# Kernel tuning notes

Measured on AMD Instinct MI355X. Metric: run time of the kernel, lower is better.

The kernel has to match this reference:

```python
import jax, jax.numpy as jnp
import numpy as np

N, E, F_IN, H, L, E_FEAT, G, OUT = 100000, 1600000, 8, 128, 4, 16, 256, 256


def setup_inputs() -> dict:
    key = jax.random.key(0)
    ks = jax.random.split(key, 12)
    inp = {
        "x": jax.random.normal(ks[0], (N, F_IN), jnp.float32),
        "edge_index": jax.random.randint(ks[1], (2, E), 0, N),
        "edge_attr": jax.random.uniform(ks[2], (E, E_FEAT), jnp.float32),
        "batch": jnp.sort(jax.random.randint(ks[3], (N,), 0, G)),
        "emb_W": jax.random.normal(ks[4], (F_IN, H), jnp.float32) / np.sqrt(F_IN),
        "emb_b": jnp.zeros((H,), jnp.float32),
        "edge_W": jax.random.normal(ks[5], (L, E_FEAT, H), jnp.float32) / np.sqrt(E_FEAT),
        "edge_b": jnp.zeros((L, H), jnp.float32),
        "nn_W": jax.random.normal(ks[6], (L, H, H), jnp.float32) / np.sqrt(H),
        "nn_b": jnp.zeros((L, H), jnp.float32),
        "bn_g": jnp.ones((L, H), jnp.float32),
        "bn_b": jnp.zeros((L, H), jnp.float32),
        "lin_W": jax.random.normal(ks[7], (H, OUT), jnp.float32) / np.sqrt(H),
        "lin_b": jnp.zeros((OUT,), jnp.float32),
    }
    return inp


def reference(x, edge_index, edge_attr, batch, emb_W, emb_b, edge_W, edge_b,
              nn_W, nn_b, bn_g, bn_b, lin_W, lin_b):
    eps_bn = 1e-5
    src, dst = edge_index[0], edge_index[1]
    h = x @ emb_W + emb_b  # node embedding [N,H]
    for l in range(L):
        e = edge_attr @ edge_W[l] + edge_b[l]          # [E,H] edge embedding
        msg = jax.nn.relu(h[src] + e)                   # gather + message
        agg = jax.ops.segment_sum(msg, dst, num_segments=N)  # scatter-add
        hc = (h + agg) @ nn_W[l] + nn_b[l]             # GINE nn (eps=0)
        mu = jnp.mean(hc, axis=0)
        var = jnp.mean((hc - mu) ** 2, axis=0)          # biased var (train BN)
        hc = (hc - mu) * jax.lax.rsqrt(var + eps_bn) * bn_g[l] + bn_b[l]
        hc = jax.nn.gelu(hc, approximate=False)
        h = h + hc                                      # 'res' residual
    out = h @ lin_W + lin_b                             # [N,OUT]
    rep = jax.ops.segment_sum(out, batch, num_segments=G)  # global_add_pool
    return rep
```

## Files before the change

### kernel.cpp

```cpp
#include <hip/hip_runtime.h>
#include <hip/hip_fp16.h>
#include <math.h>

#define GG 256

typedef __attribute__((ext_vector_type(8))) short short8;
typedef __attribute__((ext_vector_type(4))) float f32x4;
typedef _Float16 half2v __attribute__((ext_vector_type(2)));
typedef __attribute__((ext_vector_type(4))) unsigned uint4v;
typedef __attribute__((ext_vector_type(8))) unsigned uint8v;

__device__ __forceinline__ unsigned short f2bf(float x) {
  union { float f; unsigned u; } v; v.f = x;
  unsigned r = v.u + 0x7fff + ((v.u >> 16) & 1);
  return (unsigned short)(r >> 16);
}

__device__ __forceinline__ unsigned pack_h2(float a, float b) {
  __half2 h = __floats2half2_rn(a, b);
  return *(unsigned*)&h;
}

__device__ __forceinline__ float fdot2u(unsigned a, unsigned b, float c) {
  half2v av, bv;
  __builtin_memcpy(&av, &a, 4);
  __builtin_memcpy(&bv, &b, 4);
  return __builtin_amdgcn_fdot2(av, bv, c, false);
}

__device__ __forceinline__ uint4v sload4(const void* p) {
  uint4v r;
  asm volatile("s_load_dwordx4 %0, %1, 0x0"
               : "=s"(r) : "s"((unsigned long long)p));
  return r;
}
__device__ __forceinline__ uint8v sload8(const void* p) {
  uint8v r;
  asm volatile("s_load_dwordx8 %0, %1, 0x0"
               : "=s"(r) : "s"((unsigned long long)p));
  return r;
}
__device__ __forceinline__ void swait() {
  asm volatile("s_waitcnt lgkmcnt(0)" ::: "memory");
  __builtin_amdgcn_sched_barrier(0);
}

__global__ __launch_bounds__(256) void k_emb(const float* __restrict__ x,
    const float* __restrict__ W, const float* __restrict__ b,
    float* __restrict__ h, unsigned short* __restrict__ hb, int N) {
  int idx = blockIdx.x * 256 + threadIdx.x;
  if (idx >= N * 32) return;
  int n = idx >> 5, q = idx & 31;
  const float* xr = x + (size_t)n * 8;
  float xs[8];
#pragma unroll
  for (int k = 0; k < 8; ++k) xs[k] = xr[k];
  float4 acc = ((const float4*)b)[q];
#pragma unroll
  for (int k = 0; k < 8; ++k) {
    float4 w = ((const float4*)(W + (size_t)k * 128))[q];
    acc.x += xs[k] * w.x; acc.y += xs[k] * w.y;
    acc.z += xs[k] * w.z; acc.w += xs[k] * w.w;
  }
  ((float4*)h)[idx] = acc;
  ushort4 hv4 = make_ushort4(f2bf(acc.x), f2bf(acc.y), f2bf(acc.z), f2bf(acc.w));
  *(ushort4*)(hb + (size_t)idx * 4) = hv4;
}

__global__ __launch_bounds__(256) void k_wconv(const float* __restrict__ eW,
    unsigned* __restrict__ eWp) {
  int i = blockIdx.x * 256 + threadIdx.x;
  if (i >= 4096) return;
  int c = i & 127, k = (i >> 7) & 7, l = i >> 10;
  const float* base = eW + ((size_t)(l * 16 + 2 * k) * 128 + c);
  eWp[i] = pack_h2(base[0], base[128]);
}

__global__ __launch_bounds__(256) void k_nnconv(const float* __restrict__ W,
    unsigned short* __restrict__ WT) {
  int i = blockIdx.x * 256 + threadIdx.x;
  if (i >= 4 * 128 * 128) return;
  int n = i & 127, k = (i >> 7) & 127, l = i >> 14;
  WT[((size_t)(l * 128 + n)) * 128 + k] = f2bf(W[i]);
}

__global__ void k_hist(const int* __restrict__ dst, int* __restrict__ deg, int E) {
  int e = blockIdx.x * blockDim.x + threadIdx.x;
  if (e < E) atomicAdd(&deg[dst[e]], 1);
}

__global__ __launch_bounds__(256) void k_scan_reduce(const int* __restrict__ deg,
    int* __restrict__ bsum, int N) {
  __shared__ int sd[256];
  int i = blockIdx.x * 256 + threadIdx.x;
  sd[threadIdx.x] = (i < N) ? deg[i] : 0;
  __syncthreads();
  for (int s = 128; s > 0; s >>= 1) {
    if (threadIdx.x < s) sd[threadIdx.x] += sd[threadIdx.x + s];
    __syncthreads();
  }
  if (threadIdx.x == 0) bsum[blockIdx.x] = sd[0];
}

__global__ __launch_bounds__(512) void k_scan_mid(int* bsum, int nb) {
  __shared__ int sd[512];
  int t = threadIdx.x;
  int v = (t < nb) ? bsum[t] : 0;
  sd[t] = v; __syncthreads();
  for (int d = 1; d < 512; d <<= 1) {
    int xv = (t >= d) ? sd[t - d] : 0;
    __syncthreads();
    sd[t] += xv;
    __syncthreads();
  }
  if (t < nb) bsum[t] = sd[t] - v;
}

__global__ __launch_bounds__(256) void k_scan_final(const int* __restrict__ deg,
    const int* __restrict__ bsum, int* __restrict__ offs,
    int* __restrict__ cursor, int N) {
  __shared__ int sd[256];
  int t = threadIdx.x;
  int i = blockIdx.x * 256 + t;
  int v = (i < N) ? deg[i] : 0;
  sd[t] = v; __syncthreads();
  for (int d = 1; d < 256; d <<= 1) {
    int xv = (t >= d) ? sd[t - d] : 0;
    __syncthreads();
    sd[t] += xv;
    __syncthreads();
  }
  int off = bsum[blockIdx.x] + sd[t] - v;
  if (i < N) {
    offs[i] = off; cursor[i] = off;
    if (i == N - 1) offs[N] = off + v;
  }
}

__global__ void k_fill(const int* __restrict__ src, const int* __restrict__ dst,
    const float* __restrict__ attr, int* __restrict__ cursor,
    int* __restrict__ csrc, uint4* __restrict__ cattr16, int E) {
  int e = blockIdx.x * blockDim.x + threadIdx.x;
  if (e >= E) return;
  int d = dst[e];
  int pos = atomicAdd(&cursor[d], 1);
  csrc[pos] = src[e];
  const float4* a = (const float4*)(attr + (size_t)e * 16);
  float4 a0 = a[0], a1 = a[1], a2 = a[2], a3 = a[3];
  uint4 o0, o1;
  o0.x = pack_h2(a0.x, a0.y); o0.y = pack_h2(a0.z, a0.w);
  o0.z = pack_h2(a1.x, a1.y); o0.w = pack_h2(a1.z, a1.w);
  o1.x = pack_h2(a2.x, a2.y); o1.y = pack_h2(a2.z, a2.w);
  o1.z = pack_h2(a3.x, a3.y); o1.w = pack_h2(a3.z, a3.w);
  cattr16[(size_t)pos * 2] = o0;
  cattr16[(size_t)pos * 2 + 1] = o1;
}

__global__ void k_gstart(const int* __restrict__ batch, int* __restrict__ gstart,
                         int N, int Gn) {
  int i = blockIdx.x * blockDim.x + threadIdx.x;
  if (i >= N) return;
  int b = batch[i];
  if (i == 0) { for (int g = 0; g <= b; ++g) gstart[g] = 0; }
  else { int bp = batch[i - 1]; for (int g = bp + 1; g <= b; ++g) gstart[g] = i; }
  if (i == N - 1) { for (int g = b + 1; g <= Gn; ++g) gstart[g] = N; }
}

__global__ __launch_bounds__(256) void k_edge_agg(const float* __restrict__ h,
    const unsigned* __restrict__ hb32,
    const uint4* __restrict__ cattr16, const int* __restrict__ csrc,
    const int* __restrict__ offs, const unsigned* __restrict__ eWp,
    const float* __restrict__ eb, unsigned* __restrict__ hpa16,
    float* __restrict__ cstats, int N) {
  int t = threadIdx.x;
  if (blockIdx.x == 0) cstats[t] = 0.f;
  int l = t & 63;
  int wid = blockIdx.x * 4 + (t >> 6);
  int nw = gridDim.x * 4;
  uint2 wp[8];
#pragma unroll
  for (int k = 0; k < 8; ++k) wp[k] = *(const uint2*)&eWp[k * 128 + 2 * l];
  float2 bias = *(const float2*)(eb + 2 * l);
  const unsigned* hb_l = hb32 + l;

#define EDGE_SG(A, UU, AX, AY)                                              \
  {                                                                         \
    float e0 = bias.x, e1 = bias.y;                                         \
    e0 = fdot2u(A[0], wp[0].x, e0); e1 = fdot2u(A[0], wp[0].y, e1);         \
    e0 = fdot2u(A[1], wp[1].x, e0); e1 = fdot2u(A[1], wp[1].y, e1);         \
    e0 = fdot2u(A[2], wp[2].x, e0); e1 = fdot2u(A[2], wp[2].y, e1);         \
    e0 = fdot2u(A[3], wp[3].x, e0); e1 = fdot2u(A[3], wp[3].y, e1);         \
    e0 = fdot2u(A[4], wp[4].x, e0); e1 = fdot2u(A[4], wp[4].y, e1);         \
    e0 = fdot2u(A[5], wp[5].x, e0); e1 = fdot2u(A[5], wp[5].y, e1);         \
    e0 = fdot2u(A[6], wp[6].x, e0); e1 = fdot2u(A[6], wp[6].y, e1);         \
    e0 = fdot2u(A[7], wp[7].x, e0); e1 = fdot2u(A[7], wp[7].y, e1);         \
    union { unsigned uu; float ff; } c0, c1;                                \
    c0.uu = (UU) << 16; c1.uu = (UU) & 0xffff0000u;                         \
    AX += fmaxf(e0 + c0.ff, 0.f);                                           \
    AY += fmaxf(e1 + c1.ff, 0.f);                                           \
  }

#define EDGE2(JJ, UU, AX, AY)                                               \
  {                                                                         \
    uint4 q0 = cattr16[(size_t)(JJ) * 2];                                   \
    uint4 q1 = cattr16[(size_t)(JJ) * 2 + 1];                               \
    float e0 = bias.x, e1 = bias.y;                                         \
    e0 = fdot2u(q0.x, wp[0].x, e0); e1 = fdot2u(q0.x, wp[0].y, e1);         \
    e0 = fdot2u(q0.y, wp[1].x, e0); e1 = fdot2u(q0.y, wp[1].y, e1);         \
    e0 = fdot2u(q0.z, wp[2].x, e0); e1 = fdot2u(q0.z, wp[2].y, e1);         \
    e0 = fdot2u(q0.w, wp[3].x, e0); e1 = fdot2u(q0.w, wp[3].y, e1);         \
    e0 = fdot2u(q1.x, wp[4].x, e0); e1 = fdot2u(q1.x, wp[4].y, e1);         \
    e0 = fdot2u(q1.y, wp[5].x, e0); e1 = fdot2u(q1.y, wp[5].y, e1);         \
    e0 = fdot2u(q1.z, wp[6].x, e0); e1 = fdot2u(q1.z, wp[6].y, e1);         \
    e0 = fdot2u(q1.w, wp[7].x, e0); e1 = fdot2u(q1.w, wp[7].y, e1);         \
    union { unsigned uu; float ff; } c0, c1;                                \
    c0.uu = (UU) << 16; c1.uu = (UU) & 0xffff0000u;                         \
    AX += fmaxf(e0 + c0.ff, 0.f);                                           \
    AY += fmaxf(e1 + c1.ff, 0.f);                                           \
  }

  for (int n = wid; n < N; n += nw) {
    int jb = offs[n], je = offs[n + 1];
    jb = __builtin_amdgcn_readfirstlane(jb);
    je = __builtin_amdgcn_readfirstlane(je);
    float ax = 0.f, ay = 0.f, bx = 0.f, by = 0.f;
    int j = jb;
    for (; j + 4 <= je; j += 4) {
      const char* ab = (const char*)cattr16 + ((unsigned long long)(unsigned)j << 5);
      uint4v sc = sload4((const char*)csrc + ((unsigned long long)(unsigned)j << 2));
      uint8v A0 = sload8(ab);
      uint8v A1 = sload8(ab + 32);
      uint8v A2 = sload8(ab + 64);
      uint8v A3 = sload8(ab + 96);
      swait();
      const unsigned* r0 = (const unsigned*)((const char*)hb32 + ((unsigned long long)sc[0] << 8));
      const unsigned* r1 = (const unsigned*)((const char*)hb32 + ((unsigned long long)sc[1] << 8));
      const unsigned* r2 = (const unsigned*)((const char*)hb32 + ((unsigned long long)sc[2] << 8));
      const unsigned* r3 = (const unsigned*)((const char*)hb32 + ((unsigned long long)sc[3] << 8));
      unsigned u0 = r0[l], u1 = r1[l], u2 = r2[l], u3 = r3[l];
      EDGE_SG(A0, u0, ax, ay)
      EDGE_SG(A1, u1, bx, by)
      EDGE_SG(A2, u2, ax, ay)
      EDGE_SG(A3, u3, bx, by)
    }
    for (; j < je; ++j) {
      int s0 = csrc[j];
      unsigned u0 = hb_l[(size_t)s0 * 64];
      EDGE2(j, u0, ax, ay)
    }
    float2 hvv = *(const float2*)(h + (size_t)n * 128 + 2 * l);
    float rx = hvv.x + ax + bx;
    float ry = hvv.y + ay + by;
    hpa16[(size_t)n * 64 + l] = ((unsigned)f2bf(ry) << 16) | (unsigned)f2bf(rx);
  }
#undef EDGE_SG
#undef EDGE2
}

__global__ __launch_bounds__(256) void k_gemm_mfma(
    const unsigned short* __restrict__ A16, const unsigned short* __restrict__ WT16,
    const float* __restrict__ bias, float* __restrict__ hc,
    float* __restrict__ cstats, int N) {
  __shared__ short a_lds[128 * 136];
  __shared__ short w_lds[128 * 136];
  int t = threadIdx.x;
  int rowbase = blockIdx.x * 128;
  {
    int r = t >> 1;
    int off = (t & 1) * 64;
    const short* ga = (const short*)A16 + (size_t)(rowbase + r) * 128 + off;
    short* la = &a_lds[r * 136 + off];
    const short* gw = (const short*)WT16 + (size_t)r * 128 + off;
    short* lw = &w_lds[r * 136 + off];
    if (rowbase + r < N) {
#pragma unroll
      for (int jj = 0; jj < 8; ++jj)
        *(uint4*)(la + jj * 8) = *(const uint4*)(ga + jj * 8);
    } else {
#pragma unroll
      for (int jj = 0; jj < 8; ++jj)
        *(uint4*)(la + jj * 8) = make_uint4(0, 0, 0, 0);
    }
#pragma unroll
    for (int jj = 0; jj < 8; ++jj)
      *(uint4*)(lw + jj * 8) = *(const uint4*)(gw + jj * 8);
  }
  __syncthreads();
  int w = t >> 6;
  int lane = t & 63;
  int l15 = lane & 15, quad = lane >> 4;
  f32x4 acc[2][8];
#pragma unroll
  for (int rt = 0; rt < 2; ++rt)
#pragma unroll
    for (int nt = 0; nt < 8; ++nt)
      acc[rt][nt] = (f32x4){0.f, 0.f, 0.f, 0.f};
#pragma unroll
  for (int kc = 0; kc < 4; ++kc) {
    int k0 = kc * 32 + quad * 8;
    short8 af0 = *(const short8*)&a_lds[(w * 32 + l15) * 136 + k0];
    short8 af1 = *(const short8*)&a_lds[(w * 32 + 16 + l15) * 136 + k0];
#pragma unroll
    for (int nt = 0; nt < 8; ++nt) {
      short8 bf = *(const short8*)&w_lds[(nt * 16 + l15) * 136 + k0];
      acc[0][nt] = __builtin_amdgcn_mfma_f32_16x16x32_bf16(af0, bf, acc[0][nt], 0, 0, 0);
      acc[1][nt] = __builtin_amdgcn_mfma_f32_16x16x32_bf16(af1, bf, acc[1][nt], 0, 0, 0);
    }
  }
  float sA[8], sQ[8];
#pragma unroll
  for (int nt = 0; nt < 8; ++nt) { sA[nt] = 0.f; sQ[nt] = 0.f; }
#pragma unroll
  for (int nt = 0; nt < 8; ++nt) {
    int col = nt * 16 + l15;
    float bv = bias[col];
#pragma unroll
    for (int rt = 0; rt < 2; ++rt) {
      int rbase = rowbase + w * 32 + rt * 16 + quad * 4;
#pragma unroll
      for (int reg = 0; reg < 4; ++reg) {
        int row = rbase + reg;
        float v = acc[rt][nt][reg] + bv;
        if (row < N) {
          hc[(size_t)row * 128 + col] = v;
          sA[nt] += v; sQ[nt] += v * v;
        }
      }
    }
  }
#pragma unroll
  for (int nt = 0; nt < 8; ++nt) {
    sA[nt] += __shfl_xor(sA[nt], 16);
    sA[nt] += __shfl_xor(sA[nt], 32);
    sQ[nt] += __shfl_xor(sQ[nt], 16);
    sQ[nt] += __shfl_xor(sQ[nt], 32);
  }
  __syncthreads();
  float* sdA = (float*)a_lds;
  float* sdQ = (float*)w_lds;
  if (quad == 0) {
#pragma unroll
    for (int nt = 0; nt < 8; ++nt) {
      sdA[w * 128 + nt * 16 + l15] = sA[nt];
      sdQ[w * 128 + nt * 16 + l15] = sQ[nt];
    }
  }
  __syncthreads();
  if (t < 128) {
    float s = sdA[t] + sdA[128 + t] + sdA[256 + t] + sdA[384 + t];
    float s2 = sdQ[t] + sdQ[128 + t] + sdQ[256 + t] + sdQ[384 + t];
    atomicAdd(&cstats[t], s);
    atomicAdd(&cstats[128 + t], s2);
  }
}

__global__ __launch_bounds__(256) void k_bn(const float* __restrict__ hc,
    const float* __restrict__ cstats,
    const float* __restrict__ g, const float* __restrict__ bb,
    float* __restrict__ h, unsigned short* __restrict__ hb, int N) {
  int idx = blockIdx.x * 256 + threadIdx.x;
  if (idx >= N * 32) return;
  int q = idx & 31;
  float invN = 1.f / (float)N;
  float4 cs = ((const float4*)cstats)[q];
  float4 cq = ((const float4*)cstats)[q + 32];
  float4 gv = ((const float4*)g)[q];
  float4 bv = ((const float4*)bb)[q];
  float4 v = ((const float4*)hc)[idx];
  float4 hv = ((const float4*)h)[idx];
#define BN1(X)                                                      \
  { float mu = cs.X * invN;                                         \
    float var = cq.X * invN - mu * mu;                              \
    float xn = (v.X - mu) * rsqrtf(var + 1e-5f) * gv.X + bv.X;      \
    hv.X += 0.5f * xn * (1.f + erff(xn * 0.70710678118654752f)); }
  BN1(x) BN1(y) BN1(z) BN1(w)
#undef BN1
  ((float4*)h)[idx] = hv;
  if (hb) {
    ushort4 hv4 = make_ushort4(f2bf(hv.x), f2bf(hv.y), f2bf(hv.z), f2bf(hv.w));
    *(ushort4*)(hb + (size_t)idx * 4) = hv4;
  }
}

__global__ __launch_bounds__(256) void k_poolfinal(const float* __restrict__ h,
    const int* __restrict__ gstart, const float* __restrict__ W,
    const float* __restrict__ b, float* __restrict__ out) {
  int g = blockIdx.x;
  int t = threadIdx.x, c = t & 127, half = t >> 7;
  int n0 = gstart[g], n1 = gstart[g + 1];
  float s = 0.f;
  for (int n = n0 + half; n < n1; n += 2) s += h[(size_t)n * 128 + c];
  __shared__ float ls[256];
  __shared__ float pr[128];
  ls[t] = s; __syncthreads();
  if (t < 128) pr[t] = ls[t] + ls[t + 128];
  __syncthreads();
  float cnt = (float)(n1 - n0);
  float acc = cnt * b[t];
#pragma unroll 8
  for (int k = 0; k < 128; ++k) acc += pr[k] * W[(size_t)k * 256 + t];
  out[(size_t)g * 256 + t] = acc;
}

extern "C" void kernel_launch(void* const* d_in, const int* in_sizes, int n_in,
                              void* d_out, int out_size, void* d_ws, size_t ws_size,
                              hipStream_t stream) {
  const float* x     = (const float*)d_in[0];
  const int*   eidx  = (const int*)d_in[1];
  const float* eattr = (const float*)d_in[2];
  const int*   batch = (const int*)d_in[3];
  const float* embW  = (const float*)d_in[4];
  const float* embB  = (const float*)d_in[5];
  const float* edgeW = (const float*)d_in[6];
  const float* edgeB = (const float*)d_in[7];
  const float* nnW   = (const float*)d_in[8];
  const float* nnB   = (const float*)d_in[9];
  const float* bnG   = (const float*)d_in[10];
  const float* bnB   = (const float*)d_in[11];
  const float* linW  = (const float*)d_in[12];
  const float* linB  = (const float*)d_in[13];
  float* out = (float*)d_out;

  int N = in_sizes[0] / 8;
  int E = in_sizes[1] / 2;
  const int* src = eidx;
  const int* dst = eidx + E;

  char* wptr = (char*)d_ws;
  auto alloc = [&](size_t bytes) {
    char* p = wptr; wptr += (bytes + 255) & ~(size_t)255; return p;
  };
  float* h      = (float*)alloc((size_t)N * 128 * 4);
  float* hc     = (float*)alloc((size_t)N * 128 * 4);
  unsigned short* hb = (unsigned short*)alloc((size_t)N * 128 * 2);
  unsigned* hpa16 = (unsigned*)alloc((size_t)N * 64 * 4);
  uint4* cattr16 = (uint4*)alloc((size_t)E * 32);
  int*   csrc   = (int*)alloc((size_t)E * 4);
  int*   offs   = (int*)alloc((size_t)(N + 1) * 4);
  int*   cursor = (int*)alloc((size_t)N * 4);
  int*   deg    = (int*)alloc((size_t)N * 4);
  int nb = (N + 255) / 256;
  int*   bsum   = (int*)alloc((size_t)nb * 4);
  float* cstats = (float*)alloc(256 * 4);
  unsigned* eW16 = (unsigned*)alloc(4096 * 4);
  unsigned short* WT16 = (unsigned short*)alloc(4 * 128 * 128 * 2);
  int*   gstart = (int*)alloc((size_t)(GG + 1) * 4);

  int q32 = (N * 32 + 255) / 256;

  hipMemsetAsync(deg, 0, (size_t)N * 4, stream);
  k_emb<<<q32, 256, 0, stream>>>(x, embW, embB, h, hb, N);
  k_wconv<<<16, 256, 0, stream>>>(edgeW, eW16);
  k_nnconv<<<256, 256, 0, stream>>>(nnW, WT16);
  k_hist<<<(E + 255) / 256, 256, 0, stream>>>(dst, deg, E);
  k_scan_reduce<<<nb, 256, 0, stream>>>(deg, bsum, N);
  k_scan_mid<<<1, 512, 0, stream>>>(bsum, nb);
  k_scan_final<<<nb, 256, 0, stream>>>(deg, bsum, offs, cursor, N);
  k_fill<<<(E + 255) / 256, 256, 0, stream>>>(src, dst, eattr, cursor, csrc, cattr16, E);
  k_gstart<<<(N + 255) / 256, 256, 0, stream>>>(batch, gstart, N, GG);

  int gblk = (N + 127) / 128;
  for (int l = 0; l < 4; ++l) {
    k_edge_agg<<<8192, 256, 0, stream>>>(h, (const unsigned*)hb, cattr16, csrc,
        offs, eW16 + (size_t)l * 1024, edgeB + (size_t)l * 128, hpa16, cstats, N);
    k_gemm_mfma<<<gblk, 256, 0, stream>>>((const unsigned short*)hpa16,
        WT16 + (size_t)l * 128 * 128, nnB + (size_t)l * 128, hc, cstats, N);
    k_bn<<<q32, 256, 0, stream>>>(hc, cstats,
        bnG + (size_t)l * 128, bnB + (size_t)l * 128, h, (l == 3) ? nullptr : hb, N);
  }
  k_poolfinal<<<GG, 256, 0, stream>>>(h, gstart, linW, linB, out);
}
```

Baseline: 1.045 ms.

## Split CSR attr fill into coalesced convert, perm, and gather; vector-load edge attrs

Edge attribute fp16 conversion now runs as a separate coalesced pass. The CSR fill records only a permutation, and a third kernel gathers the packed 32-byte attrs into CSR order, replacing the scattered fp32 reads and writes inside the atomic fill. The scratch buffers reuse the hc and hpa16 workspace, which is enlarged when needed. In the edge aggregation kernel, attr loads move from scalar sload8 to per-lane vector loads, the loop unrolls by 8 edges with csrc prefetch, and launch bounds request 4 blocks per CU. This adds two extra kernel launches and a second pass over the attribute data.

```diff
diff --git a/kernel.cpp b/kernel.cpp
--- a/kernel.cpp
+++ b/kernel.cpp
@@ -82,6 +82,18 @@
   if (i >= 4 * 128 * 128) return;
   int n = i & 127, k = (i >> 7) & 127, l = i >> 14;
   WT[((size_t)(l * 128 + n)) * 128 + k] = f2bf(W[i]);
+}
+
+__global__ __launch_bounds__(256) void k_aconv(const float* __restrict__ attr,
+    uint4* __restrict__ attr16c, int E2) {
+  int i = blockIdx.x * 256 + threadIdx.x;
+  if (i >= E2) return;
+  float4 a0 = ((const float4*)attr)[(size_t)i * 2];
+  float4 a1 = ((const float4*)attr)[(size_t)i * 2 + 1];
+  uint4 o;
+  o.x = pack_h2(a0.x, a0.y); o.y = pack_h2(a0.z, a0.w);
+  o.z = pack_h2(a1.x, a1.y); o.w = pack_h2(a1.z, a1.w);
+  attr16c[i] = o;
 }
 
 __global__ void k_hist(const int* __restrict__ dst, int* __restrict__ deg, int E) {
@@ -137,23 +149,25 @@
   }
 }
 
-__global__ void k_fill(const int* __restrict__ src, const int* __restrict__ dst,
-    const float* __restrict__ attr, int* __restrict__ cursor,
-    int* __restrict__ csrc, uint4* __restrict__ cattr16, int E) {
+__global__ void k_fillperm(const int* __restrict__ src, const int* __restrict__ dst,
+    int* __restrict__ cursor, int* __restrict__ csrc, int* __restrict__ perm, int E) {
   int e = blockIdx.x * blockDim.x + threadIdx.x;
   if (e >= E) return;
   int d = dst[e];
   int pos = atomicAdd(&cursor[d], 1);
   csrc[pos] = src[e];
-  const float4* a = (const float4*)(attr + (size_t)e * 16);
-  float4 a0 = a[0], a1 = a[1], a2 = a[2], a3 = a[3];
-  uint4 o0, o1;
-  o0.x = pack_h2(a0.x, a0.y); o0.y = pack_h2(a0.z, a0.w);
-  o0.z = pack_h2(a1.x, a1.y); o0.w = pack_h2(a1.z, a1.w);
-  o1.x = pack_h2(a2.x, a2.y); o1.y = pack_h2(a2.z, a2.w);
-  o1.z = pack_h2(a3.x, a3.y); o1.w = pack_h2(a3.z, a3.w);
-  cattr16[(size_t)pos * 2] = o0;
-  cattr16[(size_t)pos * 2 + 1] = o1;
+  perm[pos] = e;
+}
+
+__global__ __launch_bounds__(256) void k_permgather(const int* __restrict__ perm,
+    const uint4* __restrict__ attr16c, uint4* __restrict__ cattr16, int E) {
+  int pos = blockIdx.x * 256 + threadIdx.x;
+  if (pos >= E) return;
+  int e = perm[pos];
+  uint4 a0 = attr16c[(size_t)e * 2];
+  uint4 a1 = attr16c[(size_t)e * 2 + 1];
+  cattr16[(size_t)pos * 2] = a0;
+  cattr16[(size_t)pos * 2 + 1] = a1;
 }
 
 __global__ void k_gstart(const int* __restrict__ batch, int* __restrict__ gstart,
@@ -166,7 +180,7 @@
   if (i == N - 1) { for (int g = b + 1; g <= Gn; ++g) gstart[g] = N; }
 }
 
-__global__ __launch_bounds__(256) void k_edge_agg(const float* __restrict__ h,
+__global__ __launch_bounds__(256, 4) void k_edge_agg(const float* __restrict__ h,
     const unsigned* __restrict__ hb32,
     const uint4* __restrict__ cattr16, const int* __restrict__ csrc,
     const int* __restrict__ offs, const unsigned* __restrict__ eWp,
@@ -177,84 +191,100 @@
   int l = t & 63;
   int wid = blockIdx.x * 4 + (t >> 6);
   int nw = gridDim.x * 4;
+  unsigned dz = __builtin_amdgcn_mbcnt_lo(0u, 0u);
   uint2 wp[8];
 #pragma unroll
   for (int k = 0; k < 8; ++k) wp[k] = *(const uint2*)&eWp[k * 128 + 2 * l];
   float2 bias = *(const float2*)(eb + 2 * l);
   const unsigned* hb_l = hb32 + l;
 
-#define EDGE_SG(A, UU, AX, AY)                                              \
+#define EDGE_V(P0, P1, UU, AX, AY)                                          \
   {                                                                         \
     float e0 = bias.x, e1 = bias.y;                                         \
-    e0 = fdot2u(A[0], wp[0].x, e0); e1 = fdot2u(A[0], wp[0].y, e1);         \
-    e0 = fdot2u(A[1], wp[1].x, e0); e1 = fdot2u(A[1], wp[1].y, e1);         \
-    e0 = fdot2u(A[2], wp[2].x, e0); e1 = fdot2u(A[2], wp[2].y, e1);         \
-    e0 = fdot2u(A[3], wp[3].x, e0); e1 = fdot2u(A[3], wp[3].y, e1);         \
-    e0 = fdot2u(A[4], wp[4].x, e0); e1 = fdot2u(A[4], wp[4].y, e1);         \
-    e0 = fdot2u(A[5], wp[5].x, e0); e1 = fdot2u(A[5], wp[5].y, e1);         \
-    e0 = fdot2u(A[6], wp[6].x, e0); e1 = fdot2u(A[6], wp[6].y, e1);         \
-    e0 = fdot2u(A[7], wp[7].x, e0); e1 = fdot2u(A[7], wp[7].y, e1);         \
+    e0 = fdot2u(P0.x, wp[0].x, e0); e1 = fdot2u(P0.x, wp[0].y, e1);         \
+    e0 = fdot2u(P0.y, wp[1].x, e0); e1 = fdot2u(P0.y, wp[1].y, e1);         \
+    e0 = fdot2u(P0.z, wp[2].x, e0); e1 = fdot2u(P0.z, wp[2].y, e1);         \
+    e0 = fdot2u(P0.w, wp[3].x, e0); e1 = fdot2u(P0.w, wp[3].y, e1);         \
+    e0 = fdot2u(P1.x, wp[4].x, e0); e1 = fdot2u(P1.x, wp[4].y, e1);         \
+    e0 = fdot2u(P1.y, wp[5].x, e0); e1 = fdot2u(P1.y, wp[5].y, e1);         \
+    e0 = fdot2u(P1.z, wp[6].x, e0); e1 = fdot2u(P1.z, wp[6].y, e1);         \
+    e0 = fdot2u(P1.w, wp[7].x, e0); e1 = fdot2u(P1.w, wp[7].y, e1);         \
     union { unsigned uu; float ff; } c0, c1;                                \
     c0.uu = (UU) << 16; c1.uu = (UU) & 0xffff0000u;                         \
     AX += fmaxf(e0 + c0.ff, 0.f);                                           \
     AY += fmaxf(e1 + c1.ff, 0.f);                                           \
   }
 
-#define EDGE2(JJ, UU, AX, AY)                                               \
-  {                                                                         \
-    uint4 q0 = cattr16[(size_t)(JJ) * 2];                                   \
-    uint4 q1 = cattr16[(size_t)(JJ) * 2 + 1];                               \
-    float e0 = bias.x, e1 = bias.y;                                         \
-    e0 = fdot2u(q0.x, wp[0].x, e0); e1 = fdot2u(q0.x, wp[0].y, e1);         \
-    e0 = fdot2u(q0.y, wp[1].x, e0); e1 = fdot2u(q0.y, wp[1].y, e1);         \
-    e0 = fdot2u(q0.z, wp[2].x, e0); e1 = fdot2u(q0.z, wp[2].y, e1);         \
-    e0 = fdot2u(q0.w, wp[3].x, e0); e1 = fdot2u(q0.w, wp[3].y, e1);         \
-    e0 = fdot2u(q1.x, wp[4].x, e0); e1 = fdot2u(q1.x, wp[4].y, e1);         \
-    e0 = fdot2u(q1.y, wp[5].x, e0); e1 = fdot2u(q1.y, wp[5].y, e1);         \
-    e0 = fdot2u(q1.z, wp[6].x, e0); e1 = fdot2u(q1.z, wp[6].y, e1);         \
-    e0 = fdot2u(q1.w, wp[7].x, e0); e1 = fdot2u(q1.w, wp[7].y, e1);         \
-    union { unsigned uu; float ff; } c0, c1;                                \
-    c0.uu = (UU) << 16; c1.uu = (UU) & 0xffff0000u;                         \
-    AX += fmaxf(e0 + c0.ff, 0.f);                                           \
-    AY += fmaxf(e1 + c1.ff, 0.f);                                           \
-  }
+#define LOADATTR(R0, R1, R2, R3, R4, R5, R6, R7, JJ)                        \
+  { const uint4* gp = cattr16 + (((size_t)(unsigned)(JJ)) << 1) + dz;       \
+    R0 = gp[0]; R1 = gp[1]; R2 = gp[2]; R3 = gp[3];                         \
+    R4 = gp[4]; R5 = gp[5]; R6 = gp[6]; R7 = gp[7]; }
+
+#define GATH(D, S)                                                          \
+  { const unsigned* rr = hb32 + ((size_t)(unsigned)(S)) * 64; D = rr[l]; }
 
   for (int n = wid; n < N; n += nw) {
-    int jb = offs[n], je = offs[n + 1];
-    jb = __builtin_amdgcn_readfirstlane(jb);
-    je = __builtin_amdgcn_readfirstlane(je);
+    int jb = __builtin_amdgcn_readfirstlane(offs[n]);
+    int je = __builtin_amdgcn_readfirstlane(offs[n + 1]);
     float ax = 0.f, ay = 0.f, bx = 0.f, by = 0.f;
     int j = jb;
-    for (; j + 4 <= je; j += 4) {
-      const char* ab = (const char*)cattr16 + ((unsigned long long)(unsigned)j << 5);
-      uint4v sc = sload4((const char*)csrc + ((unsigned long long)(unsigned)j << 2));
-      uint8v A0 = sload8(ab);
-      uint8v A1 = sload8(ab + 32);
-      uint8v A2 = sload8(ab + 64);
-      uint8v A3 = sload8(ab + 96);
+    if (j + 8 <= je) {
+      uint8v sc8 = sload8((const char*)csrc + ((size_t)(unsigned)j << 2));
       swait();
-      const unsigned* r0 = (const unsigned*)((const char*)hb32 + ((unsigned long long)sc[0] << 8));
-      const unsigned* r1 = (const unsigned*)((const char*)hb32 + ((unsigned long long)sc[1] << 8));
-      const unsigned* r2 = (const unsigned*)((const char*)hb32 + ((unsigned long long)sc[2] << 8));
-      const unsigned* r3 = (const unsigned*)((const char*)hb32 + ((unsigned long long)sc[3] << 8));
-      unsigned u0 = r0[l], u1 = r1[l], u2 = r2[l], u3 = r3[l];
-      EDGE_SG(A0, u0, ax, ay)
-      EDGE_SG(A1, u1, bx, by)
-      EDGE_SG(A2, u2, ax, ay)
-      EDGE_SG(A3, u3, bx, by)
+      for (;;) {
+        unsigned ua0, ua1, ua2, ua3, ub0, ub1, ub2, ub3;
+        uint4 Aa0, Aa1, Aa2, Aa3, Aa4, Aa5, Aa6, Aa7;
+        uint4 Ab0, Ab1, Ab2, Ab3, Ab4, Ab5, Ab6, Ab7;
+        GATH(ua0, sc8[0]) GATH(ua1, sc8[1]) GATH(ua2, sc8[2]) GATH(ua3, sc8[3])
+        LOADATTR(Aa0, Aa1, Aa2, Aa3, Aa4, Aa5, Aa6, Aa7, j)
+        GATH(ub0, sc8[4]) GATH(ub1, sc8[5]) GATH(ub2, sc8[6]) GATH(ub3, sc8[7])
+        LOADATTR(Ab0, Ab1, Ab2, Ab3, Ab4, Ab5, Ab6, Ab7, j + 4)
+        bool more = (j + 16 <= je);
+        uint8v sc8n;
+        if (more) sc8n = sload8((const char*)csrc + ((size_t)(unsigned)(j + 8) << 2));
+        EDGE_V(Aa0, Aa1, ua0, ax, ay)
+        EDGE_V(Aa2, Aa3, ua1, bx, by)
+        EDGE_V(Aa4, Aa5, ua2, ax, ay)
+        EDGE_V(Aa6, Aa7, ua3, bx, by)
+        EDGE_V(Ab0, Ab1, ub0, ax, ay)
+        EDGE_V(Ab2, Ab3, ub1, bx, by)
+        EDGE_V(Ab4, Ab5, ub2, ax, ay)
+        EDGE_V(Ab6, Ab7, ub3, bx, by)
+        j += 8;
+        if (!more) break;
+        swait();
+        sc8 = sc8n;
+      }
+    }
+    if (j + 4 <= je) {
+      uint4v sc4 = sload4((const char*)csrc + ((size_t)(unsigned)j << 2));
+      swait();
+      unsigned ua0, ua1, ua2, ua3;
+      uint4 Aa0, Aa1, Aa2, Aa3, Aa4, Aa5, Aa6, Aa7;
+      GATH(ua0, sc4[0]) GATH(ua1, sc4[1]) GATH(ua2, sc4[2]) GATH(ua3, sc4[3])
+      LOADATTR(Aa0, Aa1, Aa2, Aa3, Aa4, Aa5, Aa6, Aa7, j)
+      EDGE_V(Aa0, Aa1, ua0, ax, ay)
+      EDGE_V(Aa2, Aa3, ua1, bx, by)
+      EDGE_V(Aa4, Aa5, ua2, ax, ay)
+      EDGE_V(Aa6, Aa7, ua3, bx, by)
+      j += 4;
     }
     for (; j < je; ++j) {
       int s0 = csrc[j];
       unsigned u0 = hb_l[(size_t)s0 * 64];
-      EDGE2(j, u0, ax, ay)
+      uint4 P0, P1;
+      { const uint4* gp = cattr16 + (((size_t)(unsigned)j) << 1) + dz;
+        P0 = gp[0]; P1 = gp[1]; }
+      EDGE_V(P0, P1, u0, ax, ay)
     }
     float2 hvv = *(const float2*)(h + (size_t)n * 128 + 2 * l);
     float rx = hvv.x + ax + bx;
     float ry = hvv.y + ay + by;
     hpa16[(size_t)n * 64 + l] = ((unsigned)f2bf(ry) << 16) | (unsigned)f2bf(rx);
   }
-#undef EDGE_SG
-#undef EDGE2
+#undef EDGE_V
+#undef LOADATTR
+#undef GATH
 }
 
 __global__ __launch_bounds__(256) void k_gemm_mfma(
@@ -430,10 +460,14 @@
   auto alloc = [&](size_t bytes) {
     char* p = wptr; wptr += (bytes + 255) & ~(size_t)255; return p;
   };
+  size_t hc_bytes = (size_t)N * 128 * 4;
+  if ((size_t)E * 32 > hc_bytes) hc_bytes = (size_t)E * 32;
+  size_t hpa_bytes = (size_t)N * 64 * 4;
+  if ((size_t)E * 4 > hpa_bytes) hpa_bytes = (size_t)E * 4;
   float* h      = (float*)alloc((size_t)N * 128 * 4);
-  float* hc     = (float*)alloc((size_t)N * 128 * 4);
+  float* hc     = (float*)alloc(hc_bytes);
   unsigned short* hb = (unsigned short*)alloc((size_t)N * 128 * 2);
-  unsigned* hpa16 = (unsigned*)alloc((size_t)N * 64 * 4);
+  unsigned* hpa16 = (unsigned*)alloc(hpa_bytes);
   uint4* cattr16 = (uint4*)alloc((size_t)E * 32);
   int*   csrc   = (int*)alloc((size_t)E * 4);
   int*   offs   = (int*)alloc((size_t)(N + 1) * 4);
@@ -446,17 +480,22 @@
   unsigned short* WT16 = (unsigned short*)alloc(4 * 128 * 128 * 2);
   int*   gstart = (int*)alloc((size_t)(GG + 1) * 4);
 
+  uint4* attr16c = (uint4*)hc;
+  int*   perm    = (int*)hpa16;
+
   int q32 = (N * 32 + 255) / 256;
 
   hipMemsetAsync(deg, 0, (size_t)N * 4, stream);
   k_emb<<<q32, 256, 0, stream>>>(x, embW, embB, h, hb, N);
   k_wconv<<<16, 256, 0, stream>>>(edgeW, eW16);
   k_nnconv<<<256, 256, 0, stream>>>(nnW, WT16);
+  k_aconv<<<(E * 2 + 255) / 256, 256, 0, stream>>>(eattr, attr16c, E * 2);
   k_hist<<<(E + 255) / 256, 256, 0, stream>>>(dst, deg, E);
   k_scan_reduce<<<nb, 256, 0, stream>>>(deg, bsum, N);
   k_scan_mid<<<1, 512, 0, stream>>>(bsum, nb);
   k_scan_final<<<nb, 256, 0, stream>>>(deg, bsum, offs, cursor, N);
-  k_fill<<<(E + 255) / 256, 256, 0, stream>>>(src, dst, eattr, cursor, csrc, cattr16, E);
+  k_fillperm<<<(E + 255) / 256, 256, 0, stream>>>(src, dst, cursor, csrc, perm, E);
+  k_permgather<<<(E + 255) / 256, 256, 0, stream>>>(perm, attr16c, cattr16, E);
   k_gstart<<<(N + 255) / 256, 256, 0, stream>>>(batch, gstart, N, GG);
 
   int gblk = (N + 127) / 128;
```

After: 1.341 ms. +28.3%, slower.

## Double-buffer scalar loads of edge attributes and sources in edge aggregation

Applied to the files above, without the earlier changes.

Adds software pipelining to the edge-aggregation inner loop. While the current group of four edges is computed, the scalar loads for the next group of source indices and edge attributes are issued into a second register set (A/B ping-pong). The wider dwordx8 scalar loads are split into dwordx4 loads. The aim is to hide scalar-memory latency behind the gather and dot-product math, at the cost of higher SGPR pressure.

```diff
diff --git a/kernel.cpp b/kernel.cpp
--- a/kernel.cpp
+++ b/kernel.cpp
@@ -8,7 +8,6 @@
 typedef __attribute__((ext_vector_type(4))) float f32x4;
 typedef _Float16 half2v __attribute__((ext_vector_type(2)));
 typedef __attribute__((ext_vector_type(4))) unsigned uint4v;
-typedef __attribute__((ext_vector_type(8))) unsigned uint8v;
 
 __device__ __forceinline__ unsigned short f2bf(float x) {
   union { float f; unsigned u; } v; v.f = x;
@@ -31,12 +30,6 @@
 __device__ __forceinline__ uint4v sload4(const void* p) {
   uint4v r;
   asm volatile("s_load_dwordx4 %0, %1, 0x0"
-               : "=s"(r) : "s"((unsigned long long)p));
-  return r;
-}
-__device__ __forceinline__ uint8v sload8(const void* p) {
-  uint8v r;
-  asm volatile("s_load_dwordx8 %0, %1, 0x0"
                : "=s"(r) : "s"((unsigned long long)p));
   return r;
 }
@@ -183,17 +176,17 @@
   float2 bias = *(const float2*)(eb + 2 * l);
   const unsigned* hb_l = hb32 + l;
 
-#define EDGE_SG(A, UU, AX, AY)                                              \
+#define EDGE_SG(P, Q, UU, AX, AY)                                           \
   {                                                                         \
     float e0 = bias.x, e1 = bias.y;                                         \
-    e0 = fdot2u(A[0], wp[0].x, e0); e1 = fdot2u(A[0], wp[0].y, e1);         \
-    e0 = fdot2u(A[1], wp[1].x, e0); e1 = fdot2u(A[1], wp[1].y, e1);         \
-    e0 = fdot2u(A[2], wp[2].x, e0); e1 = fdot2u(A[2], wp[2].y, e1);         \
-    e0 = fdot2u(A[3], wp[3].x, e0); e1 = fdot2u(A[3], wp[3].y, e1);         \
-    e0 = fdot2u(A[4], wp[4].x, e0); e1 = fdot2u(A[4], wp[4].y, e1);         \
-    e0 = fdot2u(A[5], wp[5].x, e0); e1 = fdot2u(A[5], wp[5].y, e1);         \
-    e0 = fdot2u(A[6], wp[6].x, e0); e1 = fdot2u(A[6], wp[6].y, e1);         \
-    e0 = fdot2u(A[7], wp[7].x, e0); e1 = fdot2u(A[7], wp[7].y, e1);         \
+    e0 = fdot2u(P[0], wp[0].x, e0); e1 = fdot2u(P[0], wp[0].y, e1);         \
+    e0 = fdot2u(P[1], wp[1].x, e0); e1 = fdot2u(P[1], wp[1].y, e1);         \
+    e0 = fdot2u(P[2], wp[2].x, e0); e1 = fdot2u(P[2], wp[2].y, e1);         \
+    e0 = fdot2u(P[3], wp[3].x, e0); e1 = fdot2u(P[3], wp[3].y, e1);         \
+    e0 = fdot2u(Q[0], wp[4].x, e0); e1 = fdot2u(Q[0], wp[4].y, e1);         \
+    e0 = fdot2u(Q[1], wp[5].x, e0); e1 = fdot2u(Q[1], wp[5].y, e1);         \
+    e0 = fdot2u(Q[2], wp[6].x, e0); e1 = fdot2u(Q[2], wp[6].y, e1);         \
+    e0 = fdot2u(Q[3], wp[7].x, e0); e1 = fdot2u(Q[3], wp[7].y, e1);         \
     union { unsigned uu; float ff; } c0, c1;                                \
     c0.uu = (UU) << 16; c1.uu = (UU) & 0xffff0000u;                         \
     AX += fmaxf(e0 + c0.ff, 0.f);                                           \
@@ -219,29 +212,56 @@
     AY += fmaxf(e1 + c1.ff, 0.f);                                           \
   }
 
+#define LOADGRP(SC, A0, A1, A2, A3, A4, A5, A6, A7, JJ)                     \
+  { const char* ab_ = (const char*)cattr16 + ((size_t)(unsigned)(JJ) << 5); \
+    SC = sload4((const char*)csrc + ((size_t)(unsigned)(JJ) << 2));         \
+    A0 = sload4(ab_);       A1 = sload4(ab_ + 16);                          \
+    A2 = sload4(ab_ + 32);  A3 = sload4(ab_ + 48);                          \
+    A4 = sload4(ab_ + 64);  A5 = sload4(ab_ + 80);                          \
+    A6 = sload4(ab_ + 96);  A7 = sload4(ab_ + 112); }
+
+#define GATH4(SC, U0, U1, U2, U3)                                           \
+  { U0 = hb_l[(size_t)(SC[0]) * 64]; U1 = hb_l[(size_t)(SC[1]) * 64];       \
+    U2 = hb_l[(size_t)(SC[2]) * 64]; U3 = hb_l[(size_t)(SC[3]) * 64]; }
+
   for (int n = wid; n < N; n += nw) {
-    int jb = offs[n], je = offs[n + 1];
-    jb = __builtin_amdgcn_readfirstlane(jb);
-    je = __builtin_amdgcn_readfirstlane(je);
+    int jb = __builtin_amdgcn_readfirstlane(offs[n]);
+    int je = __builtin_amdgcn_readfirstlane(offs[n + 1]);
     float ax = 0.f, ay = 0.f, bx = 0.f, by = 0.f;
     int j = jb;
-    for (; j + 4 <= je; j += 4) {
-      const char* ab = (const char*)cattr16 + ((unsigned long long)(unsigned)j << 5);
-      uint4v sc = sload4((const char*)csrc + ((unsigned long long)(unsigned)j << 2));
-      uint8v A0 = sload8(ab);
-      uint8v A1 = sload8(ab + 32);
-      uint8v A2 = sload8(ab + 64);
-      uint8v A3 = sload8(ab + 96);
+    if (j + 4 <= je) {
+      uint4v scA, pA0, pA1, pA2, pA3, pA4, pA5, pA6, pA7;
+      uint4v scB, pB0, pB1, pB2, pB3, pB4, pB5, pB6, pB7;
+      LOADGRP(scA, pA0, pA1, pA2, pA3, pA4, pA5, pA6, pA7, j)
       swait();
-      const unsigned* r0 = (const unsigned*)((const char*)hb32 + ((unsigned long long)sc[0] << 8));
-      const unsigned* r1 = (const unsigned*)((const char*)hb32 + ((unsigned long long)sc[1] << 8));
-      const unsigned* r2 = (const unsigned*)((const char*)hb32 + ((unsigned long long)sc[2] << 8));
-      const unsigned* r3 = (const unsigned*)((const char*)hb32 + ((unsigned long long)sc[3] << 8));
-      unsigned u0 = r0[l], u1 = r1[l], u2 = r2[l], u3 = r3[l];
-      EDGE_SG(A0, u0, ax, ay)
-      EDGE_SG(A1, u1, bx, by)
-      EDGE_SG(A2, u2, ax, ay)
-      EDGE_SG(A3, u3, bx, by)
+      for (;;) {
+        {
+          unsigned u0, u1, u2, u3;
+          GATH4(scA, u0, u1, u2, u3)
+          bool more = (j + 8 <= je);
+          if (more) LOADGRP(scB, pB0, pB1, pB2, pB3, pB4, pB5, pB6, pB7, j + 4)
+          EDGE_SG(pA0, pA1, u0, ax, ay)
+          EDGE_SG(pA2, pA3, u1, bx, by)
+          EDGE_SG(pA4, pA5, u2, ax, ay)
+          EDGE_SG(pA6, pA7, u3, bx, by)
+          j += 4;
+          if (!more) break;
+          swait();
+        }
+        {
+          unsigned u0, u1, u2, u3;
+          GATH4(scB, u0, u1, u2, u3)
+          bool more = (j + 8 <= je);
+          if (more) LOADGRP(scA, pA0, pA1, pA2, pA3, pA4, pA5, pA6, pA7, j + 4)
+          EDGE_SG(pB0, pB1, u0, ax, ay)
+          EDGE_SG(pB2, pB3, u1, bx, by)
+          EDGE_SG(pB4, pB5, u2, ax, ay)
+          EDGE_SG(pB6, pB7, u3, bx, by)
+          j += 4;
+          if (!more) break;
+          swait();
+        }
+      }
     }
     for (; j < je; ++j) {
       int s0 = csrc[j];
@@ -255,6 +275,8 @@
   }
 #undef EDGE_SG
 #undef EDGE2
+#undef LOADGRP
+#undef GATH4
 }
 
 __global__ __launch_bounds__(256) void k_gemm_mfma(
```

Result: slower. 1.087 ms (+4.0%).
